# Kernel tuning notes

Measured on AMD Instinct MI355X. Metric: run time of the kernel, lower is better.

Reference implementation:

```python
import jax, jax.numpy as jnp
import numpy as np

NU, NI, D, E = 50000, 100000, 128, 500000
UMAX, IMAX = 50, 50
SQRT_D = float(np.sqrt(D))


def seg_softmax(vals, seg, n):
    # numerically stable softmax over edges grouped by segment id (sparse row softmax)
    m = jax.ops.segment_max(vals, seg, num_segments=n)
    ex = jnp.exp(vals - m[seg])
    s = jax.ops.segment_sum(ex, seg, num_segments=n)
    return ex / s[seg]


def setup_inputs() -> dict:
    key = jax.random.key(0)
    ks = jax.random.split(key, 20)
    w = lambda k: jax.random.normal(k, (D, D), dtype=jnp.float32) * 0.05
    return {
        "u_emb": jax.random.normal(ks[0], (NU, D), dtype=jnp.float32),
        "i_emb": jax.random.normal(ks[1], (NI, D), dtype=jnp.float32),
        "edge_u": jax.random.randint(ks[2], (E,), 0, NU),
        "edge_i": jax.random.randint(ks[3], (E,), 0, NI),
        "rui": jax.random.randint(ks[4], (E,), 0, UMAX),
        "riu": jax.random.randint(ks[5], (E,), 0, IMAX),
        "last_u_items": jax.random.randint(ks[6], (NU,), 0, NI),
        "last_i_users": jax.random.randint(ks[7], (NU,), 0, NU),
        "W1": w(ks[8]), "W2": w(ks[9]), "W1b": w(ks[10]), "W2b": w(ks[11]),
        "W3": w(ks[12]), "W4": w(ks[13]),
        "pV": jax.random.normal(ks[14], (UMAX, D), dtype=jnp.float32),
        "pK": jax.random.normal(ks[15], (IMAX, D), dtype=jnp.float32),
        "last_user_table": jax.random.normal(ks[16], (NU, D), dtype=jnp.float32),
        "last_item_table": jax.random.normal(ks[17], (NI, D), dtype=jnp.float32),
    }


def reference(u_emb, i_emb, edge_u, edge_i, rui, riu, last_u_items, last_i_users,
              W1, W2, W1b, W2b, W3, W4, pV, pK, last_user_table, last_item_table):
    # nn.Linear: y = x @ W.T
    um = u_emb @ W2.T            # (NU, D) user messages
    im = i_emb @ W1.T            # (NI, D) item messages
    um_e = um[edge_u]            # (E, D) gathered per edge
    im_e = im[edge_i]            # (E, D)

    # ---- long term ----
    # dense e = um @ im.T masked to edges == per-edge dot products (same math)
    e_vals = jnp.sum(um_e * im_e, axis=-1)                     # (E,)
    pVui = pV[rui]                                             # (E, D)
    pKiu = pK[riu]                                             # (E, D)
    e_ui = e_vals + jnp.sum(um_e * pVui, axis=-1)
    e_iu = e_vals + jnp.sum(im_e * pKiu, axis=-1)
    alphas = seg_softmax(e_ui / SQRT_D, edge_u, NU)            # softmax over items per user
    betas = seg_softmax(e_iu / SQRT_D, edge_i, NI)             # softmax over users per item

    umb = u_emb @ W2b.T
    imb = i_emb @ W1b.T
    # pass_messages: out[row] = sum_e alpha_e * (messages[col_e] + p_e)
    hLu = jax.ops.segment_sum(alphas[:, None] * (imb[edge_i] + pKiu), edge_u, num_segments=NU)
    hLi = jax.ops.segment_sum(betas[:, None] * (umb[edge_u] + pVui), edge_i, num_segments=NI)

    # ---- short term ----
    li = last_item_table[last_u_items] @ W3.T                  # (NU, D)
    lu = last_user_table[last_i_users] @ W4.T                  # (NU, D)
    a_vals = jnp.sum(li[edge_u] * im_e, axis=-1)               # (E,)
    b_vals = jnp.sum(lu[edge_u] * im_e, axis=-1)               # (E,)
    alphas_s = seg_softmax(a_vals / SQRT_D, edge_u, NU)
    betas_s = seg_softmax(b_vals / SQRT_D, edge_i, NI)
    # p = ones -> messages + 1
    hSu = jax.ops.segment_sum(alphas_s[:, None] * (im_e + 1.0), edge_u, num_segments=NU)
    hSi = jax.ops.segment_sum(betas_s[:, None] * (um_e + 1.0), edge_i, num_segments=NI)

    return (hLu, hSu, hLi, hSi)
```

## Files before the change

### kernel.cpp

```cpp
#include <hip/hip_runtime.h>
#include <hip/hip_bf16.h>
#include <math.h>

#define D_ 128
#define INV_SQRT_D 0.08838834764831845f
#define SCAN_CH 16
#define SCAN_TILE (256 * SCAN_CH)

typedef __bf16 bf16x8 __attribute__((ext_vector_type(8)));
typedef __bf16 bf16x4 __attribute__((ext_vector_type(4)));
typedef float f32x4 __attribute__((ext_vector_type(4)));

struct W6 { const float* p[6]; };

__device__ __forceinline__ void unpack4(bf16x4 v, float* f) {
    const uint32_t* u = (const uint32_t*)&v;
#pragma unroll
    for (int i = 0; i < 2; i++) {
        uint32_t w = u[i];
        f[2 * i]     = __uint_as_float(w << 16);
        f[2 * i + 1] = __uint_as_float(w & 0xffff0000u);
    }
}

__global__ __launch_bounds__(256) void cvt_weights(W6 w, __bf16* __restrict__ out) {
    int idx = blockIdx.x * 256 + threadIdx.x;
    if (idx >= 6 * 16384) return;
    out[idx] = (__bf16)w.p[idx >> 14][idx & 16383];
}

__global__ __launch_bounds__(256) void cvt2(const float* __restrict__ a, const float* __restrict__ b,
                                            __bf16* __restrict__ oa, __bf16* __restrict__ ob, int n) {
    int idx = blockIdx.x * 256 + threadIdx.x;
    if (idx < n) { oa[idx] = (__bf16)a[idx]; ob[idx] = (__bf16)b[idx]; }
}

__global__ __launch_bounds__(256) void gemm_xwt(const float* __restrict__ X,
                                                const int* __restrict__ gidx,
                                                const __bf16* __restrict__ Wb,
                                                __bf16* __restrict__ Y, int ystride, int rows) {
    int lane = threadIdx.x & 63;
    int wave = threadIdx.x >> 6;
    int row0 = blockIdx.x * 64 + wave * 16;
    if (row0 >= rows) return;
    int l16 = lane & 15, kh = lane >> 4;
    int ar = row0 + l16;
    int arc = ar < rows ? ar : rows - 1;
    long srcrow = gidx ? (long)gidx[arc] : (long)arc;
    const float* arow = X + (size_t)srcrow * D_;

    f32x4 acc[8] = {};
#pragma unroll
    for (int k0 = 0; k0 < D_; k0 += 32) {
        int kk = k0 + kh * 8;
        float4 a0 = *(const float4*)(arow + kk);
        float4 a1 = *(const float4*)(arow + kk + 4);
        bf16x8 af;
        af[0] = (__bf16)a0.x; af[1] = (__bf16)a0.y; af[2] = (__bf16)a0.z; af[3] = (__bf16)a0.w;
        af[4] = (__bf16)a1.x; af[5] = (__bf16)a1.y; af[6] = (__bf16)a1.z; af[7] = (__bf16)a1.w;
#pragma unroll
        for (int cb = 0; cb < 8; cb++) {
            bf16x8 bf = *(const bf16x8*)(Wb + (size_t)(cb * 16 + l16) * D_ + kk);
            acc[cb] = __builtin_amdgcn_mfma_f32_16x16x32_bf16(af, bf, acc[cb], 0, 0, 0);
        }
    }
#pragma unroll
    for (int cb = 0; cb < 8; cb++) {
#pragma unroll
        for (int j = 0; j < 4; j++) {
            int r = row0 + kh * 4 + j;
            if (r < rows) Y[(size_t)r * ystride + cb * 16 + l16] = (__bf16)acc[cb][j];
        }
    }
}

__global__ __launch_bounds__(256) void gemm_dual(const float* __restrict__ X,
                                                 const __bf16* __restrict__ WA,
                                                 const __bf16* __restrict__ WB,
                                                 __bf16* __restrict__ YA, int sA,
                                                 __bf16* __restrict__ YB, int sB, int rows) {
    int lane = threadIdx.x & 63;
    int wave = threadIdx.x >> 6;
    int row0 = blockIdx.x * 64 + wave * 16;
    if (row0 >= rows) return;
    int l16 = lane & 15, kh = lane >> 4;
    int ar = row0 + l16;
    int arc = ar < rows ? ar : rows - 1;
    const float* arow = X + (size_t)arc * D_;

    f32x4 accA[8] = {}, accB[8] = {};
#pragma unroll
    for (int k0 = 0; k0 < D_; k0 += 32) {
        int kk = k0 + kh * 8;
        float4 a0 = *(const float4*)(arow + kk);
        float4 a1 = *(const float4*)(arow + kk + 4);
        bf16x8 af;
        af[0] = (__bf16)a0.x; af[1] = (__bf16)a0.y; af[2] = (__bf16)a0.z; af[3] = (__bf16)a0.w;
        af[4] = (__bf16)a1.x; af[5] = (__bf16)a1.y; af[6] = (__bf16)a1.z; af[7] = (__bf16)a1.w;
#pragma unroll
        for (int cb = 0; cb < 8; cb++) {
            bf16x8 bfA = *(const bf16x8*)(WA + (size_t)(cb * 16 + l16) * D_ + kk);
            accA[cb] = __builtin_amdgcn_mfma_f32_16x16x32_bf16(af, bfA, accA[cb], 0, 0, 0);
            bf16x8 bfB = *(const bf16x8*)(WB + (size_t)(cb * 16 + l16) * D_ + kk);
            accB[cb] = __builtin_amdgcn_mfma_f32_16x16x32_bf16(af, bfB, accB[cb], 0, 0, 0);
        }
    }
#pragma unroll
    for (int cb = 0; cb < 8; cb++) {
#pragma unroll
        for (int j = 0; j < 4; j++) {
            int r = row0 + kh * 4 + j;
            if (r < rows) {
                YA[(size_t)r * sA + cb * 16 + l16] = (__bf16)accA[cb][j];
                YB[(size_t)r * sB + cb * 16 + l16] = (__bf16)accB[cb][j];
            }
        }
    }
}

__global__ __launch_bounds__(256) void gemm_pvk(const __bf16* __restrict__ Xb, int xstride,
                                                const __bf16* __restrict__ Pb,
                                                float* __restrict__ Y, int rows, int ncols) {
    int lane = threadIdx.x & 63;
    int wave = threadIdx.x >> 6;
    int row0 = blockIdx.x * 64 + wave * 16;
    if (row0 >= rows) return;
    int l16 = lane & 15, kh = lane >> 4;
    int ar = row0 + l16;
    int arc = ar < rows ? ar : rows - 1;
    const __bf16* arow = Xb + (size_t)arc * xstride;

    f32x4 acc[4] = {};
#pragma unroll
    for (int k0 = 0; k0 < D_; k0 += 32) {
        int kk = k0 + kh * 8;
        bf16x8 af = *(const bf16x8*)(arow + kk);
#pragma unroll
        for (int cb = 0; cb < 4; cb++) {
            int br = cb * 16 + l16;
            if (br >= ncols) br = ncols - 1;
            bf16x8 bf = *(const bf16x8*)(Pb + (size_t)br * D_ + kk);
            acc[cb] = __builtin_amdgcn_mfma_f32_16x16x32_bf16(af, bf, acc[cb], 0, 0, 0);
        }
    }
#pragma unroll
    for (int cb = 0; cb < 4; cb++) {
        int col = cb * 16 + l16;
        if (col >= ncols) continue;
#pragma unroll
        for (int j = 0; j < 4; j++) {
            int r = row0 + kh * 4 + j;
            if (r < rows) Y[(size_t)r * ncols + col] = acc[cb][j];
        }
    }
}

__global__ __launch_bounds__(256) void hist2(const int* __restrict__ eu, const int* __restrict__ ei,
                                             int* __restrict__ cnt_all, int nu, int E) {
    int e = blockIdx.x * 256 + threadIdx.x;
    if (e < E) {
        atomicAdd(&cnt_all[eu[e]], 1);
        atomicAdd(&cnt_all[nu + ei[e]], 1);
    }
}

__global__ __launch_bounds__(256) void scan_phaseA(const int* __restrict__ cnt, int* __restrict__ part, int n) {
    __shared__ int wsum[4];
    int t = threadIdx.x, lane = t & 63, w = t >> 6;
    int i0 = blockIdx.x * SCAN_TILE + t * SCAN_CH;
    int tot = 0;
#pragma unroll
    for (int j = 0; j < SCAN_CH; j++) tot += (i0 + j < n) ? cnt[i0 + j] : 0;
#pragma unroll
    for (int d = 32; d; d >>= 1) tot += __shfl_xor(tot, d);
    if (lane == 0) wsum[w] = tot;
    __syncthreads();
    if (t == 0) part[blockIdx.x] = wsum[0] + wsum[1] + wsum[2] + wsum[3];
}

__global__ __launch_bounds__(1024) void scan_phaseB(int* __restrict__ part, int nb,
                                                    int* __restrict__ off, int n) {
    __shared__ int wsum[16];
    int t = threadIdx.x, lane = t & 63, w = t >> 6;
    int v = (t < nb) ? part[t] : 0;
    int x = v;
#pragma unroll
    for (int d = 1; d < 64; d <<= 1) {
        int y = __shfl_up(x, d);
        if (lane >= d) x += y;
    }
    if (lane == 63) wsum[w] = x;
    __syncthreads();
    int wbase = 0;
    for (int ww = 0; ww < w; ww++) wbase += wsum[ww];
    if (t < nb) part[t] = wbase + x - v;
    if (t == 1023) off[n] = wbase + x;
}

__global__ __launch_bounds__(256) void scan_phaseC(const int* __restrict__ cnt, const int* __restrict__ part,
                                                   int* __restrict__ off, int* __restrict__ pos, int n) {
    __shared__ int wsum[4];
    int t = threadIdx.x, lane = t & 63, w = t >> 6;
    int i0 = blockIdx.x * SCAN_TILE + t * SCAN_CH;
    int loc[SCAN_CH];
    int tot = 0;
#pragma unroll
    for (int j = 0; j < SCAN_CH; j++) {
        int v = (i0 + j < n) ? cnt[i0 + j] : 0;
        loc[j] = tot; tot += v;
    }
    int x = tot;
#pragma unroll
    for (int d = 1; d < 64; d <<= 1) {
        int y = __shfl_up(x, d);
        if (lane >= d) x += y;
    }
    if (lane == 63) wsum[w] = x;
    __syncthreads();
    int wbase = 0;
    for (int ww = 0; ww < w; ww++) wbase += wsum[ww];
    int excl = part[blockIdx.x] + wbase + x - tot;
#pragma unroll
    for (int j = 0; j < SCAN_CH; j++) {
        if (i0 + j < n) { off[i0 + j] = excl + loc[j]; pos[i0 + j] = excl + loc[j]; }
    }
}

__global__ __launch_bounds__(256) void scatter2(const int* __restrict__ eu, const int* __restrict__ ei,
                                                int* __restrict__ pos_all, int* __restrict__ list_all,
                                                int nu, int E) {
    int e = blockIdx.x * 256 + threadIdx.x;
    if (e < E) {
        int pu = atomicAdd(&pos_all[eu[e]], 1);
        list_all[pu] = e;
        int pi = atomicAdd(&pos_all[nu + ei[e]], 1);
        list_all[pi] = e;
    }
}

__global__ __launch_bounds__(256) void user_fused(const int* __restrict__ off_all, const int* __restrict__ list_all,
                                                  const int* __restrict__ ei, const int* __restrict__ rui,
                                                  const int* __restrict__ riu,
                                                  const __bf16* __restrict__ i_rec,
                                                  const __bf16* __restrict__ u_rec,
                                                  const __bf16* __restrict__ li,
                                                  const __bf16* __restrict__ pKb,
                                                  const float* __restrict__ upv,
                                                  float* __restrict__ hLu, float* __restrict__ hSu,
                                                  int nu, int umax) {
    int u = blockIdx.x * 4 + (threadIdx.x >> 6);
    if (u >= nu) return;
    int lane = threadIdx.x & 63;
    int g = lane >> 5, l32 = lane & 31;
    int off = off_all[u], n = off_all[u + 1] - off;
    if (n == 0) {
        if (lane < 32) {
            ((float4*)(hLu + (size_t)u * D_))[l32] = make_float4(0.f, 0.f, 0.f, 0.f);
            ((float4*)(hSu + (size_t)u * D_))[l32] = make_float4(0.f, 0.f, 0.f, 0.f);
        }
        return;
    }
    float um4[4], li4[4];
    unpack4(*(const bf16x4*)(u_rec + (size_t)u * 384 + l32 * 4), um4);
    unpack4(*(const bf16x4*)(li + (size_t)u * D_ + l32 * 4), li4);
    const float* upv_row = upv + (size_t)u * umax;

    float m1 = -INFINITY, s1 = 0.f, a1[4] = {};
    float m2 = -INFINITY, s2 = 0.f, a2[4] = {};
    for (int i = g; i < n; i += 2) {
        int e = list_all[off + i];
        int item = ei[e];
        const __bf16* ib = i_rec + (size_t)item * 256;
        bf16x4 imv  = ((const bf16x4*)ib)[l32];
        bf16x4 imbv = ((const bf16x4*)(ib + 128))[l32];
        bf16x4 pkv  = ((const bf16x4*)(pKb + (size_t)riu[e] * D_))[l32];
        float uv = upv_row[rui[e]];
        float fim[4], fimb[4], fpk[4];
        unpack4(imv, fim); unpack4(imbv, fimb); unpack4(pkv, fpk);
        float d1 = 0.f, d2 = 0.f;
#pragma unroll
        for (int j = 0; j < 4; j++) {
            d1 = fmaf(um4[j], fim[j], d1);
            d2 = fmaf(li4[j], fim[j], d2);
        }
#pragma unroll
        for (int d = 16; d; d >>= 1) {
            d1 += __shfl_xor(d1, d);
            d2 += __shfl_xor(d2, d);
        }
        float lg1 = (d1 + uv) * INV_SQRT_D;
        float lg2 = d2 * INV_SQRT_D;
        float mn = fmaxf(m1, lg1);
        float r  = __expf(m1 - mn);
        float w  = __expf(lg1 - mn);
        s1 = s1 * r + w; m1 = mn;
#pragma unroll
        for (int j = 0; j < 4; j++) a1[j] = fmaf(a1[j], r, w * (fimb[j] + fpk[j]));
        mn = fmaxf(m2, lg2);
        r  = __expf(m2 - mn);
        w  = __expf(lg2 - mn);
        s2 = s2 * r + w; m2 = mn;
#pragma unroll
        for (int j = 0; j < 4; j++) a2[j] = fmaf(a2[j], r, w * (fim[j] + 1.f));
    }
    float mo = __shfl_xor(m1, 32);
    float mm = fmaxf(m1, mo);
    float r  = __expf(m1 - mm);
    s1 *= r;
#pragma unroll
    for (int j = 0; j < 4; j++) a1[j] *= r;
    s1 += __shfl_xor(s1, 32);
#pragma unroll
    for (int j = 0; j < 4; j++) a1[j] += __shfl_xor(a1[j], 32);
    mo = __shfl_xor(m2, 32);
    mm = fmaxf(m2, mo);
    r  = __expf(m2 - mm);
    s2 *= r;
#pragma unroll
    for (int j = 0; j < 4; j++) a2[j] *= r;
    s2 += __shfl_xor(s2, 32);
#pragma unroll
    for (int j = 0; j < 4; j++) a2[j] += __shfl_xor(a2[j], 32);

    float inv1 = 1.f / s1, inv2 = 1.f / s2;
    if (lane < 32) {
        ((float4*)(hLu + (size_t)u * D_))[l32] = make_float4(a1[0] * inv1, a1[1] * inv1, a1[2] * inv1, a1[3] * inv1);
        ((float4*)(hSu + (size_t)u * D_))[l32] = make_float4(a2[0] * inv2, a2[1] * inv2, a2[2] * inv2, a2[3] * inv2);
    }
}

__global__ __launch_bounds__(256) void item_fused(const int* __restrict__ off_all, const int* __restrict__ list_all,
                                                  const int* __restrict__ eu, const int* __restrict__ rui,
                                                  const int* __restrict__ riu,
                                                  const __bf16* __restrict__ i_rec,
                                                  const __bf16* __restrict__ u_rec,
                                                  const __bf16* __restrict__ pVb,
                                                  const float* __restrict__ ipk,
                                                  float* __restrict__ hLi, float* __restrict__ hSi,
                                                  int nu, int ni, int imax) {
    int it = blockIdx.x * 4 + (threadIdx.x >> 6);
    if (it >= ni) return;
    int lane = threadIdx.x & 63;
    int g = lane >> 5, l32 = lane & 31;
    int off = off_all[nu + it], n = off_all[nu + it + 1] - off;
    if (n == 0) {
        if (lane < 32) {
            ((float4*)(hLi + (size_t)it * D_))[l32] = make_float4(0.f, 0.f, 0.f, 0.f);
            ((float4*)(hSi + (size_t)it * D_))[l32] = make_float4(0.f, 0.f, 0.f, 0.f);
        }
        return;
    }
    float im4[4];
    unpack4(*(const bf16x4*)(i_rec + (size_t)it * 256 + l32 * 4), im4);
    const float* ipk_row = ipk + (size_t)it * imax;

    float m1 = -INFINITY, s1 = 0.f, a1[4] = {};
    float m2 = -INFINITY, s2 = 0.f, a2[4] = {};
    for (int i = g; i < n; i += 2) {
        int e = list_all[off + i];
        int user = eu[e];
        const __bf16* ub = u_rec + (size_t)user * 384;
        bf16x4 umv  = ((const bf16x4*)ub)[l32];
        bf16x4 umbv = ((const bf16x4*)(ub + 128))[l32];
        bf16x4 luv  = ((const bf16x4*)(ub + 256))[l32];
        bf16x4 pvv  = ((const bf16x4*)(pVb + (size_t)rui[e] * D_))[l32];
        float iv = ipk_row[riu[e]];
        float fum[4], fumb[4], flu[4], fpv[4];
        unpack4(umv, fum); unpack4(umbv, fumb); unpack4(luv, flu); unpack4(pvv, fpv);
        float d1 = 0.f, d2 = 0.f;
#pragma unroll
        for (int j = 0; j < 4; j++) {
            d1 = fmaf(fum[j], im4[j], d1);
            d2 = fmaf(flu[j], im4[j], d2);
        }
#pragma unroll
        for (int d = 16; d; d >>= 1) {
            d1 += __shfl_xor(d1, d);
            d2 += __shfl_xor(d2, d);
        }
        float lg1 = (d1 + iv) * INV_SQRT_D;
        float lg2 = d2 * INV_SQRT_D;
        float mn = fmaxf(m1, lg1);
        float r  = __expf(m1 - mn);
        float w  = __expf(lg1 - mn);
        s1 = s1 * r + w; m1 = mn;
#pragma unroll
        for (int j = 0; j < 4; j++) a1[j] = fmaf(a1[j], r, w * (fumb[j] + fpv[j]));
        mn = fmaxf(m2, lg2);
        r  = __expf(m2 - mn);
        w  = __expf(lg2 - mn);
        s2 = s2 * r + w; m2 = mn;
#pragma unroll
        for (int j = 0; j < 4; j++) a2[j] = fmaf(a2[j], r, w * (fum[j] + 1.f));
    }
    float mo = __shfl_xor(m1, 32);
    float mm = fmaxf(m1, mo);
    float r  = __expf(m1 - mm);
    s1 *= r;
#pragma unroll
    for (int j = 0; j < 4; j++) a1[j] *= r;
    s1 += __shfl_xor(s1, 32);
#pragma unroll
    for (int j = 0; j < 4; j++) a1[j] += __shfl_xor(a1[j], 32);
    mo = __shfl_xor(m2, 32);
    mm = fmaxf(m2, mo);
    r  = __expf(m2 - mm);
    s2 *= r;
#pragma unroll
    for (int j = 0; j < 4; j++) a2[j] *= r;
    s2 += __shfl_xor(s2, 32);
#pragma unroll
    for (int j = 0; j < 4; j++) a2[j] += __shfl_xor(a2[j], 32);

    float inv1 = 1.f / s1, inv2 = 1.f / s2;
    if (lane < 32) {
        ((float4*)(hLi + (size_t)it * D_))[l32] = make_float4(a1[0] * inv1, a1[1] * inv1, a1[2] * inv1, a1[3] * inv1);
        ((float4*)(hSi + (size_t)it * D_))[l32] = make_float4(a2[0] * inv2, a2[1] * inv2, a2[2] * inv2, a2[3] * inv2);
    }
}

extern "C" void kernel_launch(void* const* d_in, const int* in_sizes, int n_in,
                              void* d_out, int out_size, void* d_ws, size_t ws_size,
                              hipStream_t stream) {
    (void)n_in; (void)out_size; (void)ws_size;
    const float* u_emb = (const float*)d_in[0];
    const float* i_emb = (const float*)d_in[1];
    const int* edge_u = (const int*)d_in[2];
    const int* edge_i = (const int*)d_in[3];
    const int* rui = (const int*)d_in[4];
    const int* riu = (const int*)d_in[5];
    const int* last_u_items = (const int*)d_in[6];
    const int* last_i_users = (const int*)d_in[7];
    const float* W1  = (const float*)d_in[8];
    const float* W2  = (const float*)d_in[9];
    const float* W1b = (const float*)d_in[10];
    const float* W2b = (const float*)d_in[11];
    const float* W3  = (const float*)d_in[12];
    const float* W4  = (const float*)d_in[13];
    const float* pV  = (const float*)d_in[14];
    const float* pK  = (const float*)d_in[15];
    const float* last_user_table = (const float*)d_in[16];
    const float* last_item_table = (const float*)d_in[17];

    const int NU = in_sizes[0] / D_;
    const int NI = in_sizes[1] / D_;
    const int E  = in_sizes[2];
    const int UMAXr = in_sizes[14] / D_;
    const int IMAXr = in_sizes[15] / D_;
    const int NSEG = NU + NI;

    size_t cur = 0;
    auto alloc = [&](size_t bytes) -> void* {
        void* p = (char*)d_ws + cur;
        cur += (bytes + 255) & ~(size_t)255;
        return p;
    };

    __bf16* Wb    = (__bf16*)alloc(6 * 16384 * sizeof(__bf16));
    __bf16* pVb   = (__bf16*)alloc((size_t)UMAXr * D_ * 2);
    __bf16* pKb   = (__bf16*)alloc((size_t)IMAXr * D_ * 2);
    __bf16* i_rec = (__bf16*)alloc((size_t)NI * 256 * 2);
    __bf16* u_rec = (__bf16*)alloc((size_t)NU * 384 * 2);
    __bf16* li_bf = (__bf16*)alloc((size_t)NU * D_ * 2);
    float* upv   = (float*)alloc((size_t)NU * UMAXr * 4);
    float* ipk   = (float*)alloc((size_t)NI * IMAXr * 4);
    int* cnt_all  = (int*)alloc((size_t)NSEG * 4);
    int* off_all  = (int*)alloc((size_t)(NSEG + 1) * 4);
    int* pos_all  = (int*)alloc((size_t)NSEG * 4);
    int* list_all = (int*)alloc((size_t)2 * E * 4);
    int* parts    = (int*)alloc(1024 * 4);

    float* out = (float*)d_out;
    float* hLu = out;
    float* hSu = out + (size_t)NU * D_;
    float* hLi = out + (size_t)2 * NU * D_;
    float* hSi = out + (size_t)2 * NU * D_ + (size_t)NI * D_;

    W6 w6;
    w6.p[0] = W1; w6.p[1] = W2; w6.p[2] = W1b; w6.p[3] = W2b; w6.p[4] = W3; w6.p[5] = W4;
    cvt_weights<<<(6 * 16384 + 255) / 256, 256, 0, stream>>>(w6, Wb);
    cvt2<<<(UMAXr * D_ + 255) / 256, 256, 0, stream>>>(pV, pK, pVb, pKb, UMAXr * D_);

    hipMemsetAsync(cnt_all, 0, (size_t)NSEG * 4, stream);
    hist2<<<(E + 255) / 256, 256, 0, stream>>>(edge_u, edge_i, cnt_all, NU, E);
    int nb = (NSEG + SCAN_TILE - 1) / SCAN_TILE;
    scan_phaseA<<<nb, 256, 0, stream>>>(cnt_all, parts, NSEG);
    scan_phaseB<<<1, 1024, 0, stream>>>(parts, nb, off_all, NSEG);
    scan_phaseC<<<nb, 256, 0, stream>>>(cnt_all, parts, off_all, pos_all, NSEG);
    scatter2<<<(E + 255) / 256, 256, 0, stream>>>(edge_u, edge_i, pos_all, list_all, NU, E);

    int gu = (NU + 63) / 64, gi = (NI + 63) / 64;
    gemm_dual<<<gi, 256, 0, stream>>>(i_emb, Wb + 0 * 16384, Wb + 2 * 16384,
                                      i_rec + 0, 256, i_rec + 128, 256, NI);
    gemm_dual<<<gu, 256, 0, stream>>>(u_emb, Wb + 1 * 16384, Wb + 3 * 16384,
                                      u_rec + 0, 384, u_rec + 128, 384, NU);
    gemm_xwt<<<gu, 256, 0, stream>>>(last_item_table, last_u_items, Wb + 4 * 16384, li_bf, 128, NU);
    gemm_xwt<<<gu, 256, 0, stream>>>(last_user_table, last_i_users, Wb + 5 * 16384, u_rec + 256, 384, NU);

    gemm_pvk<<<gu, 256, 0, stream>>>(u_rec, 384, pVb, upv, NU, UMAXr);
    gemm_pvk<<<gi, 256, 0, stream>>>(i_rec, 256, pKb, ipk, NI, IMAXr);

    user_fused<<<(NU + 3) / 4, 256, 0, stream>>>(off_all, list_all, edge_i, rui, riu,
                                                 i_rec, u_rec, li_bf, pKb, upv, hLu, hSu, NU, UMAXr);
    item_fused<<<(NI + 3) / 4, 256, 0, stream>>>(off_all, list_all, edge_u, rui, riu,
                                                 i_rec, u_rec, pVb, ipk, hLi, hSi, NU, NI, IMAXr);
}
```

Baseline: 497.7 us.

## Share per-edge logits between user and item passes and drop online softmax max

The user pass now computes the long-term and both short-term dot products per edge and writes the two item-side logits to a per-edge buffer. The item pass reads that buffer instead of gathering its own item row and recomputing the dots. Each 64-lane wave now processes four edges at once with 16 lanes × 8 bf16 elements. The running-max rescaling is removed in favour of a plain exp-sum, and the 1/sqrt(D) scale is folded into the pvk GEMM output and the preloaded query rows. The constant +1 message term is applied once after normalisation. This removes redundant gathers and exp work, but adds an E-sized buffer, and skipping max subtraction risks overflow if logits ever become large.

```diff
diff --git a/kernel.cpp b/kernel.cpp
--- a/kernel.cpp
+++ b/kernel.cpp
@@ -8,15 +8,14 @@
 #define SCAN_TILE (256 * SCAN_CH)
 
 typedef __bf16 bf16x8 __attribute__((ext_vector_type(8)));
-typedef __bf16 bf16x4 __attribute__((ext_vector_type(4)));
 typedef float f32x4 __attribute__((ext_vector_type(4)));
 
 struct W6 { const float* p[6]; };
 
-__device__ __forceinline__ void unpack4(bf16x4 v, float* f) {
+__device__ __forceinline__ void unpack8(bf16x8 v, float* f) {
     const uint32_t* u = (const uint32_t*)&v;
 #pragma unroll
-    for (int i = 0; i < 2; i++) {
+    for (int i = 0; i < 4; i++) {
         uint32_t w = u[i];
         f[2 * i]     = __uint_as_float(w << 16);
         f[2 * i + 1] = __uint_as_float(w & 0xffff0000u);
@@ -150,7 +149,7 @@
 #pragma unroll
         for (int j = 0; j < 4; j++) {
             int r = row0 + kh * 4 + j;
-            if (r < rows) Y[(size_t)r * ncols + col] = acc[cb][j];
+            if (r < rows) Y[(size_t)r * ncols + col] = acc[cb][j] * INV_SQRT_D;
         }
     }
 }
@@ -243,179 +242,148 @@
                                                   const int* __restrict__ riu,
                                                   const __bf16* __restrict__ i_rec,
                                                   const __bf16* __restrict__ u_rec,
-                                                  const __bf16* __restrict__ li,
+                                                  const __bf16* __restrict__ li_t,
+                                                  const __bf16* __restrict__ lu_t,
                                                   const __bf16* __restrict__ pKb,
                                                   const float* __restrict__ upv,
+                                                  float2* __restrict__ mb_val,
                                                   float* __restrict__ hLu, float* __restrict__ hSu,
                                                   int nu, int umax) {
     int u = blockIdx.x * 4 + (threadIdx.x >> 6);
     if (u >= nu) return;
     int lane = threadIdx.x & 63;
-    int g = lane >> 5, l32 = lane & 31;
+    int g = lane >> 4, l16 = lane & 15;
     int off = off_all[u], n = off_all[u + 1] - off;
     if (n == 0) {
-        if (lane < 32) {
-            ((float4*)(hLu + (size_t)u * D_))[l32] = make_float4(0.f, 0.f, 0.f, 0.f);
-            ((float4*)(hSu + (size_t)u * D_))[l32] = make_float4(0.f, 0.f, 0.f, 0.f);
+        if (lane < 16) {
+            float4 z = make_float4(0.f, 0.f, 0.f, 0.f);
+            ((float4*)(hLu + (size_t)u * D_ + l16 * 8))[0] = z;
+            ((float4*)(hLu + (size_t)u * D_ + l16 * 8))[1] = z;
+            ((float4*)(hSu + (size_t)u * D_ + l16 * 8))[0] = z;
+            ((float4*)(hSu + (size_t)u * D_ + l16 * 8))[1] = z;
         }
         return;
     }
-    float um4[4], li4[4];
-    unpack4(*(const bf16x4*)(u_rec + (size_t)u * 384 + l32 * 4), um4);
-    unpack4(*(const bf16x4*)(li + (size_t)u * D_ + l32 * 4), li4);
+    float um8[8], li8[8], lu8[8];
+    unpack8(((const bf16x8*)(u_rec + (size_t)u * 256))[l16], um8);
+    unpack8(((const bf16x8*)(li_t + (size_t)u * D_))[l16], li8);
+    unpack8(((const bf16x8*)(lu_t + (size_t)u * D_))[l16], lu8);
+#pragma unroll
+    for (int j = 0; j < 8; j++) { um8[j] *= INV_SQRT_D; li8[j] *= INV_SQRT_D; lu8[j] *= INV_SQRT_D; }
     const float* upv_row = upv + (size_t)u * umax;
 
-    float m1 = -INFINITY, s1 = 0.f, a1[4] = {};
-    float m2 = -INFINITY, s2 = 0.f, a2[4] = {};
-    for (int i = g; i < n; i += 2) {
+    float s1 = 0.f, s2 = 0.f, a1[8] = {}, a2[8] = {};
+    for (int i = g; i < n; i += 4) {
         int e = list_all[off + i];
         int item = ei[e];
         const __bf16* ib = i_rec + (size_t)item * 256;
-        bf16x4 imv  = ((const bf16x4*)ib)[l32];
-        bf16x4 imbv = ((const bf16x4*)(ib + 128))[l32];
-        bf16x4 pkv  = ((const bf16x4*)(pKb + (size_t)riu[e] * D_))[l32];
-        float uv = upv_row[rui[e]];
-        float fim[4], fimb[4], fpk[4];
-        unpack4(imv, fim); unpack4(imbv, fimb); unpack4(pkv, fpk);
-        float d1 = 0.f, d2 = 0.f;
-#pragma unroll
-        for (int j = 0; j < 4; j++) {
-            d1 = fmaf(um4[j], fim[j], d1);
-            d2 = fmaf(li4[j], fim[j], d2);
-        }
-#pragma unroll
-        for (int d = 16; d; d >>= 1) {
+        bf16x8 imv  = ((const bf16x8*)ib)[l16];
+        bf16x8 imbv = ((const bf16x8*)(ib + 128))[l16];
+        bf16x8 pkv  = ((const bf16x8*)(pKb + (size_t)riu[e] * D_))[l16];
+        float fim[8], fimb[8], fpk[8];
+        unpack8(imv, fim); unpack8(imbv, fimb); unpack8(pkv, fpk);
+        float d1 = 0.f, d2 = 0.f, d3 = 0.f;
+#pragma unroll
+        for (int j = 0; j < 8; j++) {
+            d1 = fmaf(um8[j], fim[j], d1);
+            d2 = fmaf(li8[j], fim[j], d2);
+            d3 = fmaf(lu8[j], fim[j], d3);
+        }
+#pragma unroll
+        for (int d = 1; d < 16; d <<= 1) {
             d1 += __shfl_xor(d1, d);
             d2 += __shfl_xor(d2, d);
-        }
-        float lg1 = (d1 + uv) * INV_SQRT_D;
-        float lg2 = d2 * INV_SQRT_D;
-        float mn = fmaxf(m1, lg1);
-        float r  = __expf(m1 - mn);
-        float w  = __expf(lg1 - mn);
-        s1 = s1 * r + w; m1 = mn;
-#pragma unroll
-        for (int j = 0; j < 4; j++) a1[j] = fmaf(a1[j], r, w * (fimb[j] + fpk[j]));
-        mn = fmaxf(m2, lg2);
-        r  = __expf(m2 - mn);
-        w  = __expf(lg2 - mn);
-        s2 = s2 * r + w; m2 = mn;
-#pragma unroll
-        for (int j = 0; j < 4; j++) a2[j] = fmaf(a2[j], r, w * (fim[j] + 1.f));
-    }
-    float mo = __shfl_xor(m1, 32);
-    float mm = fmaxf(m1, mo);
-    float r  = __expf(m1 - mm);
-    s1 *= r;
-#pragma unroll
-    for (int j = 0; j < 4; j++) a1[j] *= r;
-    s1 += __shfl_xor(s1, 32);
-#pragma unroll
-    for (int j = 0; j < 4; j++) a1[j] += __shfl_xor(a1[j], 32);
-    mo = __shfl_xor(m2, 32);
-    mm = fmaxf(m2, mo);
-    r  = __expf(m2 - mm);
-    s2 *= r;
-#pragma unroll
-    for (int j = 0; j < 4; j++) a2[j] *= r;
-    s2 += __shfl_xor(s2, 32);
-#pragma unroll
-    for (int j = 0; j < 4; j++) a2[j] += __shfl_xor(a2[j], 32);
-
-    float inv1 = 1.f / s1, inv2 = 1.f / s2;
-    if (lane < 32) {
-        ((float4*)(hLu + (size_t)u * D_))[l32] = make_float4(a1[0] * inv1, a1[1] * inv1, a1[2] * inv1, a1[3] * inv1);
-        ((float4*)(hSu + (size_t)u * D_))[l32] = make_float4(a2[0] * inv2, a2[1] * inv2, a2[2] * inv2, a2[3] * inv2);
+            d3 += __shfl_xor(d3, d);
+        }
+        if (l16 == 0) mb_val[e] = make_float2(d1, d3);
+        float w1 = __expf(d1 + upv_row[rui[e]]);
+        float w2 = __expf(d2);
+        s1 += w1; s2 += w2;
+#pragma unroll
+        for (int j = 0; j < 8; j++) {
+            a1[j] = fmaf(w1, fimb[j] + fpk[j], a1[j]);
+            a2[j] = fmaf(w2, fim[j], a2[j]);
+        }
+    }
+#pragma unroll
+    for (int d = 16; d < 64; d <<= 1) {
+        s1 += __shfl_xor(s1, d); s2 += __shfl_xor(s2, d);
+#pragma unroll
+        for (int j = 0; j < 8; j++) {
+            a1[j] += __shfl_xor(a1[j], d);
+            a2[j] += __shfl_xor(a2[j], d);
+        }
+    }
+    if (lane < 16) {
+        float inv1 = 1.f / s1, inv2 = 1.f / s2;
+        ((float4*)(hLu + (size_t)u * D_ + l16 * 8))[0] = make_float4(a1[0]*inv1, a1[1]*inv1, a1[2]*inv1, a1[3]*inv1);
+        ((float4*)(hLu + (size_t)u * D_ + l16 * 8))[1] = make_float4(a1[4]*inv1, a1[5]*inv1, a1[6]*inv1, a1[7]*inv1);
+        ((float4*)(hSu + (size_t)u * D_ + l16 * 8))[0] = make_float4(a2[0]*inv2+1.f, a2[1]*inv2+1.f, a2[2]*inv2+1.f, a2[3]*inv2+1.f);
+        ((float4*)(hSu + (size_t)u * D_ + l16 * 8))[1] = make_float4(a2[4]*inv2+1.f, a2[5]*inv2+1.f, a2[6]*inv2+1.f, a2[7]*inv2+1.f);
     }
 }
 
 __global__ __launch_bounds__(256) void item_fused(const int* __restrict__ off_all, const int* __restrict__ list_all,
                                                   const int* __restrict__ eu, const int* __restrict__ rui,
                                                   const int* __restrict__ riu,
-                                                  const __bf16* __restrict__ i_rec,
                                                   const __bf16* __restrict__ u_rec,
                                                   const __bf16* __restrict__ pVb,
                                                   const float* __restrict__ ipk,
+                                                  const float2* __restrict__ mb_val,
                                                   float* __restrict__ hLi, float* __restrict__ hSi,
                                                   int nu, int ni, int imax) {
     int it = blockIdx.x * 4 + (threadIdx.x >> 6);
     if (it >= ni) return;
     int lane = threadIdx.x & 63;
-    int g = lane >> 5, l32 = lane & 31;
+    int g = lane >> 4, l16 = lane & 15;
     int off = off_all[nu + it], n = off_all[nu + it + 1] - off;
     if (n == 0) {
-        if (lane < 32) {
-            ((float4*)(hLi + (size_t)it * D_))[l32] = make_float4(0.f, 0.f, 0.f, 0.f);
-            ((float4*)(hSi + (size_t)it * D_))[l32] = make_float4(0.f, 0.f, 0.f, 0.f);
+        if (lane < 16) {
+            float4 z = make_float4(0.f, 0.f, 0.f, 0.f);
+            ((float4*)(hLi + (size_t)it * D_ + l16 * 8))[0] = z;
+            ((float4*)(hLi + (size_t)it * D_ + l16 * 8))[1] = z;
+            ((float4*)(hSi + (size_t)it * D_ + l16 * 8))[0] = z;
+            ((float4*)(hSi + (size_t)it * D_ + l16 * 8))[1] = z;
         }
         return;
     }
-    float im4[4];
-    unpack4(*(const bf16x4*)(i_rec + (size_t)it * 256 + l32 * 4), im4);
     const float* ipk_row = ipk + (size_t)it * imax;
 
-    float m1 = -INFINITY, s1 = 0.f, a1[4] = {};
-    float m2 = -INFINITY, s2 = 0.f, a2[4] = {};
-    for (int i = g; i < n; i += 2) {
+    float s1 = 0.f, s2 = 0.f, a1[8] = {}, a2[8] = {};
+    for (int i = g; i < n; i += 4) {
         int e = list_all[off + i];
         int user = eu[e];
-        const __bf16* ub = u_rec + (size_t)user * 384;
-        bf16x4 umv  = ((const bf16x4*)ub)[l32];
-        bf16x4 umbv = ((const bf16x4*)(ub + 128))[l32];
-        bf16x4 luv  = ((const bf16x4*)(ub + 256))[l32];
-        bf16x4 pvv  = ((const bf16x4*)(pVb + (size_t)rui[e] * D_))[l32];
-        float iv = ipk_row[riu[e]];
-        float fum[4], fumb[4], flu[4], fpv[4];
-        unpack4(umv, fum); unpack4(umbv, fumb); unpack4(luv, flu); unpack4(pvv, fpv);
-        float d1 = 0.f, d2 = 0.f;
-#pragma unroll
-        for (int j = 0; j < 4; j++) {
-            d1 = fmaf(fum[j], im4[j], d1);
-            d2 = fmaf(flu[j], im4[j], d2);
-        }
-#pragma unroll
-        for (int d = 16; d; d >>= 1) {
-            d1 += __shfl_xor(d1, d);
-            d2 += __shfl_xor(d2, d);
-        }
-        float lg1 = (d1 + iv) * INV_SQRT_D;
-        float lg2 = d2 * INV_SQRT_D;
-        float mn = fmaxf(m1, lg1);
-        float r  = __expf(m1 - mn);
-        float w  = __expf(lg1 - mn);
-        s1 = s1 * r + w; m1 = mn;
-#pragma unroll
-        for (int j = 0; j < 4; j++) a1[j] = fmaf(a1[j], r, w * (fumb[j] + fpv[j]));
-        mn = fmaxf(m2, lg2);
-        r  = __expf(m2 - mn);
-        w  = __expf(lg2 - mn);
-        s2 = s2 * r + w; m2 = mn;
-#pragma unroll
-        for (int j = 0; j < 4; j++) a2[j] = fmaf(a2[j], r, w * (fum[j] + 1.f));
-    }
-    float mo = __shfl_xor(m1, 32);
-    float mm = fmaxf(m1, mo);
-    float r  = __expf(m1 - mm);
-    s1 *= r;
-#pragma unroll
-    for (int j = 0; j < 4; j++) a1[j] *= r;
-    s1 += __shfl_xor(s1, 32);
-#pragma unroll
-    for (int j = 0; j < 4; j++) a1[j] += __shfl_xor(a1[j], 32);
-    mo = __shfl_xor(m2, 32);
-    mm = fmaxf(m2, mo);
-    r  = __expf(m2 - mm);
-    s2 *= r;
-#pragma unroll
-    for (int j = 0; j < 4; j++) a2[j] *= r;
-    s2 += __shfl_xor(s2, 32);
-#pragma unroll
-    for (int j = 0; j < 4; j++) a2[j] += __shfl_xor(a2[j], 32);
-
-    float inv1 = 1.f / s1, inv2 = 1.f / s2;
-    if (lane < 32) {
-        ((float4*)(hLi + (size_t)it * D_))[l32] = make_float4(a1[0] * inv1, a1[1] * inv1, a1[2] * inv1, a1[3] * inv1);
-        ((float4*)(hSi + (size_t)it * D_))[l32] = make_float4(a2[0] * inv2, a2[1] * inv2, a2[2] * inv2, a2[3] * inv2);
+        float2 mb = mb_val[e];
+        const __bf16* ub = u_rec + (size_t)user * 256;
+        bf16x8 umv  = ((const bf16x8*)ub)[l16];
+        bf16x8 umbv = ((const bf16x8*)(ub + 128))[l16];
+        bf16x8 pvv  = ((const bf16x8*)(pVb + (size_t)rui[e] * D_))[l16];
+        float fum[8], fumb[8], fpv[8];
+        unpack8(umv, fum); unpack8(umbv, fumb); unpack8(pvv, fpv);
+        float w1 = __expf(mb.x + ipk_row[riu[e]]);
+        float w2 = __expf(mb.y);
+        s1 += w1; s2 += w2;
+#pragma unroll
+        for (int j = 0; j < 8; j++) {
+            a1[j] = fmaf(w1, fumb[j] + fpv[j], a1[j]);
+            a2[j] = fmaf(w2, fum[j], a2[j]);
+        }
+    }
+#pragma unroll
+    for (int d = 16; d < 64; d <<= 1) {
+        s1 += __shfl_xor(s1, d); s2 += __shfl_xor(s2, d);
+#pragma unroll
+        for (int j = 0; j < 8; j++) {
+            a1[j] += __shfl_xor(a1[j], d);
+            a2[j] += __shfl_xor(a2[j], d);
+        }
+    }
+    if (lane < 16) {
+        float inv1 = 1.f / s1, inv2 = 1.f / s2;
+        ((float4*)(hLi + (size_t)it * D_ + l16 * 8))[0] = make_float4(a1[0]*inv1, a1[1]*inv1, a1[2]*inv1, a1[3]*inv1);
+        ((float4*)(hLi + (size_t)it * D_ + l16 * 8))[1] = make_float4(a1[4]*inv1, a1[5]*inv1, a1[6]*inv1, a1[7]*inv1);
+        ((float4*)(hSi + (size_t)it * D_ + l16 * 8))[0] = make_float4(a2[0]*inv2+1.f, a2[1]*inv2+1.f, a2[2]*inv2+1.f, a2[3]*inv2+1.f);
+        ((float4*)(hSi + (size_t)it * D_ + l16 * 8))[1] = make_float4(a2[4]*inv2+1.f, a2[5]*inv2+1.f, a2[6]*inv2+1.f, a2[7]*inv2+1.f);
     }
 }
 
@@ -460,10 +428,12 @@
     __bf16* pVb   = (__bf16*)alloc((size_t)UMAXr * D_ * 2);
     __bf16* pKb   = (__bf16*)alloc((size_t)IMAXr * D_ * 2);
     __bf16* i_rec = (__bf16*)alloc((size_t)NI * 256 * 2);
-    __bf16* u_rec = (__bf16*)alloc((size_t)NU * 384 * 2);
+    __bf16* u_rec = (__bf16*)alloc((size_t)NU * 256 * 2);
     __bf16* li_bf = (__bf16*)alloc((size_t)NU * D_ * 2);
-    float* upv   = (float*)alloc((size_t)NU * UMAXr * 4);
-    float* ipk   = (float*)alloc((size_t)NI * IMAXr * 4);
+    __bf16* lu_bf = (__bf16*)alloc((size_t)NU * D_ * 2);
+    float* upv    = (float*)alloc((size_t)NU * UMAXr * 4);
+    float* ipk    = (float*)alloc((size_t)NI * IMAXr * 4);
+    float2* mb_val = (float2*)alloc((size_t)E * 8);
     int* cnt_all  = (int*)alloc((size_t)NSEG * 4);
     int* off_all  = (int*)alloc((size_t)(NSEG + 1) * 4);
     int* pos_all  = (int*)alloc((size_t)NSEG * 4);
@@ -493,15 +463,17 @@
     gemm_dual<<<gi, 256, 0, stream>>>(i_emb, Wb + 0 * 16384, Wb + 2 * 16384,
                                       i_rec + 0, 256, i_rec + 128, 256, NI);
     gemm_dual<<<gu, 256, 0, stream>>>(u_emb, Wb + 1 * 16384, Wb + 3 * 16384,
-                                      u_rec + 0, 384, u_rec + 128, 384, NU);
+                                      u_rec + 0, 256, u_rec + 128, 256, NU);
     gemm_xwt<<<gu, 256, 0, stream>>>(last_item_table, last_u_items, Wb + 4 * 16384, li_bf, 128, NU);
-    gemm_xwt<<<gu, 256, 0, stream>>>(last_user_table, last_i_users, Wb + 5 * 16384, u_rec + 256, 384, NU);
-
-    gemm_pvk<<<gu, 256, 0, stream>>>(u_rec, 384, pVb, upv, NU, UMAXr);
+    gemm_xwt<<<gu, 256, 0, stream>>>(last_user_table, last_i_users, Wb + 5 * 16384, lu_bf, 128, NU);
+
+    gemm_pvk<<<gu, 256, 0, stream>>>(u_rec, 256, pVb, upv, NU, UMAXr);
     gemm_pvk<<<gi, 256, 0, stream>>>(i_rec, 256, pKb, ipk, NI, IMAXr);
 
     user_fused<<<(NU + 3) / 4, 256, 0, stream>>>(off_all, list_all, edge_i, rui, riu,
-                                                 i_rec, u_rec, li_bf, pKb, upv, hLu, hSu, NU, UMAXr);
+                                                 i_rec, u_rec, li_bf, lu_bf, pKb, upv, mb_val,
+                                                 hLu, hSu, NU, UMAXr);
     item_fused<<<(NI + 3) / 4, 256, 0, stream>>>(off_all, list_all, edge_u, rui, riu,
-                                                 i_rec, u_rec, pVb, ipk, hLi, hSi, NU, NI, IMAXr);
-}
+                                                 u_rec, pVb, ipk, mb_val,
+                                                 hLi, hSi, NU, NI, IMAXr);
+}
```

Measured after the change: 495.5 us. About the same (-0.4%).
